# Optimization experiments

Measured on AMD Instinct MI355X. Metric: run time of the kernel, lower is better.

## Reference

```python
import jax, jax.numpy as jnp
import numpy as np

NUM_ITEMS = 100000
HIDDEN = 128
NNZ = 1600000


def setup_inputs() -> dict:
    key = jax.random.key(0)
    k1, k2, k3, k4, k5, k6 = jax.random.split(key, 6)
    item_embedding_table = jax.random.normal(k1, (NUM_ITEMS, HIDDEN), dtype=jnp.float32)
    adj_rows = jnp.sort(jax.random.randint(k2, (NNZ,), 0, NUM_ITEMS, dtype=jnp.int32))
    adj_cols = jax.random.randint(k3, (NNZ,), 0, NUM_ITEMS, dtype=jnp.int32)
    adj_vals = jax.random.uniform(k4, (NNZ,), dtype=jnp.float32)
    # nn.Linear default init (uniform in +-1/sqrt(fan_in)) approximated by scaled normal
    W_weight = jax.random.normal(k5, (HIDDEN, HIDDEN), dtype=jnp.float32) / np.sqrt(HIDDEN)
    W_bias = jax.random.normal(k6, (HIDDEN,), dtype=jnp.float32) * 0.01
    return {
        "item_embedding_table": item_embedding_table,
        "adj_rows": adj_rows,
        "adj_cols": adj_cols,
        "adj_vals": adj_vals,
        "W_weight": W_weight,
        "W_bias": W_bias,
    }


def reference(item_embedding_table, adj_rows, adj_cols, adj_vals, W_weight, W_bias):
    # support = W(x): x @ W^T + b   (nn.Linear convention: weight [out, in])
    support = jnp.einsum("nd,hd->nh", item_embedding_table, W_weight) + W_bias  # [N, H]
    # output = sparse_coo(adj) @ support, via gather + segment-sum scatter
    msgs = adj_vals[:, None] * support[adj_cols]  # [nnz, H]
    output = jax.ops.segment_sum(msgs, adj_rows, num_segments=NUM_ITEMS)  # [N, H]
    return output
```

## Files before the change

### kernel.cpp

```cpp
#include <hip/hip_runtime.h>

#define N_ITEMS 100000
#define HID 128
#define NNZ_T 1600000

typedef unsigned short ushort_t;
typedef unsigned int uint_t;
typedef short bf16x8 __attribute__((ext_vector_type(8)));
typedef float f32x4 __attribute__((ext_vector_type(4)));

static __device__ __forceinline__ ushort_t f32_to_bf16(float f) {
    uint_t u = __float_as_uint(f);
    uint_t r = (u + 0x7FFFu + ((u >> 16) & 1u)) >> 16;
    return (ushort_t)r;
}

__global__ void prep_w(const float* __restrict__ W, ushort_t* __restrict__ Wb) {
    int i = blockIdx.x * blockDim.x + threadIdx.x;
    Wb[i] = f32_to_bf16(W[i]);
}

__global__ void build_rowptr(const int* __restrict__ rows, int* __restrict__ row_ptr) {
    int r = blockIdx.x * blockDim.x + threadIdx.x;
    if (r > N_ITEMS) return;
    int lo = 0, hi = NNZ_T;
    while (lo < hi) {
        int mid = (lo + hi) >> 1;
        if (rows[mid] < r) lo = mid + 1; else hi = mid;
    }
    row_ptr[r] = lo;
}

__global__ __launch_bounds__(256) void gemm_mfma(
    const float* __restrict__ X, const ushort_t* __restrict__ Wb,
    const float* __restrict__ bias, ushort_t* __restrict__ S) {
    const int lane = threadIdx.x & 63;
    const int wave = threadIdx.x >> 6;
    const int m = lane & 15;
    const int q = lane >> 4;
    const int row0 = blockIdx.x * 64 + wave * 16;

    int arow = row0 + m;
    if (arow >= N_ITEMS) arow = N_ITEMS - 1;

    f32x4 acc[8] = {};

#pragma unroll
    for (int kb = 0; kb < 4; ++kb) {
        const int k0 = kb * 32 + q * 8;
        float4 a0 = *(const float4*)&X[(size_t)arow * HID + k0];
        float4 a1 = *(const float4*)&X[(size_t)arow * HID + k0 + 4];
        bf16x8 af;
        af[0] = (short)f32_to_bf16(a0.x); af[1] = (short)f32_to_bf16(a0.y);
        af[2] = (short)f32_to_bf16(a0.z); af[3] = (short)f32_to_bf16(a0.w);
        af[4] = (short)f32_to_bf16(a1.x); af[5] = (short)f32_to_bf16(a1.y);
        af[6] = (short)f32_to_bf16(a1.z); af[7] = (short)f32_to_bf16(a1.w);
#pragma unroll
        for (int nt = 0; nt < 8; ++nt) {
            bf16x8 bfr = *(const bf16x8*)&Wb[(size_t)(nt * 16 + m) * HID + k0];
            acc[nt] = __builtin_amdgcn_mfma_f32_16x16x32_bf16(af, bfr, acc[nt], 0, 0, 0);
        }
    }

#pragma unroll
    for (int nt = 0; nt < 8; ++nt) {
        const int col = nt * 16 + m;
        const float bv = bias[col];
#pragma unroll
        for (int r = 0; r < 4; ++r) {
            const int row = row0 + q * 4 + r;
            if (row < N_ITEMS)
                S[(size_t)row * HID + col] = f32_to_bf16(acc[nt][r] + bv);
        }
    }
}

__global__ __launch_bounds__(256) void spmm_csr(
    const int* __restrict__ cols, const float* __restrict__ vals,
    const int* __restrict__ row_ptr, const ushort_t* __restrict__ S,
    float* __restrict__ out) {
    const int lane = threadIdx.x & 63;
    const int row = blockIdx.x * 4 + (int)__builtin_amdgcn_readfirstlane(threadIdx.x >> 6);
    if (row >= N_ITEMS) return;

    const int p0 = row_ptr[row];
    const int p1 = row_ptr[row + 1];

    float2 acc = make_float2(0.f, 0.f);
    int p = p0;
    for (; p + 8 <= p1; p += 8) {
        uint_t u[8]; float v[8];
#pragma unroll
        for (int j = 0; j < 8; ++j) {
            int c = cols[p + j];
            v[j] = vals[p + j];
            u[j] = *(const uint_t*)&S[(size_t)c * HID + 2 * lane];
        }
#pragma unroll
        for (int j = 0; j < 8; ++j) {
            acc.x = fmaf(v[j], __uint_as_float(u[j] << 16), acc.x);
            acc.y = fmaf(v[j], __uint_as_float(u[j] & 0xFFFF0000u), acc.y);
        }
    }
    for (; p < p1; ++p) {
        int c = cols[p];
        float v = vals[p];
        uint_t u = *(const uint_t*)&S[(size_t)c * HID + 2 * lane];
        acc.x = fmaf(v, __uint_as_float(u << 16), acc.x);
        acc.y = fmaf(v, __uint_as_float(u & 0xFFFF0000u), acc.y);
    }
    *(float2*)&out[(size_t)row * HID + 2 * lane] = acc;
}

extern "C" void kernel_launch(void* const* d_in, const int* in_sizes, int n_in,
                              void* d_out, int out_size, void* d_ws, size_t ws_size,
                              hipStream_t stream) {
    const float* X    = (const float*)d_in[0];
    const int*   rows = (const int*)  d_in[1];
    const int*   cols = (const int*)  d_in[2];
    const float* vals = (const float*)d_in[3];
    const float* W    = (const float*)d_in[4];
    const float* bias = (const float*)d_in[5];
    float* out = (float*)d_out;

    ushort_t* Wb      = (ushort_t*)d_ws;
    ushort_t* S       = Wb + HID * HID;
    int*      row_ptr = (int*)(S + (size_t)N_ITEMS * HID);

    prep_w<<<(HID * HID) / 256, 256, 0, stream>>>(W, Wb);
    build_rowptr<<<(N_ITEMS + 256) / 256, 256, 0, stream>>>(rows, row_ptr);
    gemm_mfma<<<(N_ITEMS + 63) / 64, 256, 0, stream>>>(X, Wb, bias, S);
    spmm_csr<<<(N_ITEMS + 3) / 4, 256, 0, stream>>>(cols, vals, row_ptr, S, out);
}
```

Before: 222.6 us.

## Fuse weight cast and rowptr build into GEMM, process two rows per SpMM wave

Drops the separate W-to-bf16 and row_ptr kernels. The GEMM now converts fp32 W inline, and the binary-search rowptr build runs in extra blocks of the same launch, so two kernels become one. The MFMA operands are swapped so each lane holds contiguous output columns, which lets the epilogue write packed 8-byte stores with a float4 bias load. The SpMM kernel handles two adjacent rows per wave with interleaved, clamped and masked gathers, giving more memory-level parallelism. The cost is redundant W conversion in every GEMM block and wasted gathers when the two row lengths differ.

```diff
diff --git a/kernel.cpp b/kernel.cpp
--- a/kernel.cpp
+++ b/kernel.cpp
@@ -3,6 +3,8 @@
 #define N_ITEMS 100000
 #define HID 128
 #define NNZ_T 1600000
+#define GEMM_BLOCKS 1563
+#define RP_BLOCKS 391
 
 typedef unsigned short ushort_t;
 typedef unsigned int uint_t;
@@ -15,25 +17,23 @@
     return (ushort_t)r;
 }
 
-__global__ void prep_w(const float* __restrict__ W, ushort_t* __restrict__ Wb) {
-    int i = blockIdx.x * blockDim.x + threadIdx.x;
-    Wb[i] = f32_to_bf16(W[i]);
-}
+__global__ __launch_bounds__(256) void gemm_rowptr(
+    const float* __restrict__ X, const float* __restrict__ W,
+    const float* __restrict__ bias, const int* __restrict__ rows,
+    ushort_t* __restrict__ S, int* __restrict__ row_ptr) {
 
-__global__ void build_rowptr(const int* __restrict__ rows, int* __restrict__ row_ptr) {
-    int r = blockIdx.x * blockDim.x + threadIdx.x;
-    if (r > N_ITEMS) return;
-    int lo = 0, hi = NNZ_T;
-    while (lo < hi) {
-        int mid = (lo + hi) >> 1;
-        if (rows[mid] < r) lo = mid + 1; else hi = mid;
+    if (blockIdx.x >= GEMM_BLOCKS) {
+        int r = (blockIdx.x - GEMM_BLOCKS) * 256 + threadIdx.x;
+        if (r > N_ITEMS) return;
+        int lo = 0, hi = NNZ_T;
+        while (lo < hi) {
+            int mid = (lo + hi) >> 1;
+            if (rows[mid] < r) lo = mid + 1; else hi = mid;
+        }
+        row_ptr[r] = lo;
+        return;
     }
-    row_ptr[r] = lo;
-}
 
-__global__ __launch_bounds__(256) void gemm_mfma(
-    const float* __restrict__ X, const ushort_t* __restrict__ Wb,
-    const float* __restrict__ bias, ushort_t* __restrict__ S) {
     const int lane = threadIdx.x & 63;
     const int wave = threadIdx.x >> 6;
     const int m = lane & 15;
@@ -50,28 +50,38 @@
         const int k0 = kb * 32 + q * 8;
         float4 a0 = *(const float4*)&X[(size_t)arow * HID + k0];
         float4 a1 = *(const float4*)&X[(size_t)arow * HID + k0 + 4];
-        bf16x8 af;
-        af[0] = (short)f32_to_bf16(a0.x); af[1] = (short)f32_to_bf16(a0.y);
-        af[2] = (short)f32_to_bf16(a0.z); af[3] = (short)f32_to_bf16(a0.w);
-        af[4] = (short)f32_to_bf16(a1.x); af[5] = (short)f32_to_bf16(a1.y);
-        af[6] = (short)f32_to_bf16(a1.z); af[7] = (short)f32_to_bf16(a1.w);
+        bf16x8 xf;
+        xf[0] = (short)f32_to_bf16(a0.x); xf[1] = (short)f32_to_bf16(a0.y);
+        xf[2] = (short)f32_to_bf16(a0.z); xf[3] = (short)f32_to_bf16(a0.w);
+        xf[4] = (short)f32_to_bf16(a1.x); xf[5] = (short)f32_to_bf16(a1.y);
+        xf[6] = (short)f32_to_bf16(a1.z); xf[7] = (short)f32_to_bf16(a1.w);
 #pragma unroll
         for (int nt = 0; nt < 8; ++nt) {
-            bf16x8 bfr = *(const bf16x8*)&Wb[(size_t)(nt * 16 + m) * HID + k0];
-            acc[nt] = __builtin_amdgcn_mfma_f32_16x16x32_bf16(af, bfr, acc[nt], 0, 0, 0);
+            float4 w0 = *(const float4*)&W[(size_t)(nt * 16 + m) * HID + k0];
+            float4 w1 = *(const float4*)&W[(size_t)(nt * 16 + m) * HID + k0 + 4];
+            bf16x8 wf;
+            wf[0] = (short)f32_to_bf16(w0.x); wf[1] = (short)f32_to_bf16(w0.y);
+            wf[2] = (short)f32_to_bf16(w0.z); wf[3] = (short)f32_to_bf16(w0.w);
+            wf[4] = (short)f32_to_bf16(w1.x); wf[5] = (short)f32_to_bf16(w1.y);
+            wf[6] = (short)f32_to_bf16(w1.z); wf[7] = (short)f32_to_bf16(w1.w);
+            acc[nt] = __builtin_amdgcn_mfma_f32_16x16x32_bf16(wf, xf, acc[nt], 0, 0, 0);
         }
     }
 
+    const int srow = row0 + m;
+    const bool ok = srow < N_ITEMS;
 #pragma unroll
     for (int nt = 0; nt < 8; ++nt) {
-        const int col = nt * 16 + m;
-        const float bv = bias[col];
-#pragma unroll
-        for (int r = 0; r < 4; ++r) {
-            const int row = row0 + q * 4 + r;
-            if (row < N_ITEMS)
-                S[(size_t)row * HID + col] = f32_to_bf16(acc[nt][r] + bv);
-        }
+        const int c0 = nt * 16 + q * 4;
+        float4 bv = *(const float4*)&bias[c0];
+        ushort_t h0 = f32_to_bf16(acc[nt][0] + bv.x);
+        ushort_t h1 = f32_to_bf16(acc[nt][1] + bv.y);
+        ushort_t h2 = f32_to_bf16(acc[nt][2] + bv.z);
+        ushort_t h3 = f32_to_bf16(acc[nt][3] + bv.w);
+        uint2 pk;
+        pk.x = (uint_t)h0 | ((uint_t)h1 << 16);
+        pk.y = (uint_t)h2 | ((uint_t)h3 << 16);
+        if (ok) *(uint2*)&S[(size_t)srow * HID + c0] = pk;
     }
 }
 
@@ -80,36 +90,47 @@
     const int* __restrict__ row_ptr, const ushort_t* __restrict__ S,
     float* __restrict__ out) {
     const int lane = threadIdx.x & 63;
-    const int row = blockIdx.x * 4 + (int)__builtin_amdgcn_readfirstlane(threadIdx.x >> 6);
-    if (row >= N_ITEMS) return;
+    const int wid = blockIdx.x * 4 + ((threadIdx.x >> 6) & 3);
+    const int r0 = wid * 2;
+    if (r0 >= N_ITEMS) return;
 
-    const int p0 = row_ptr[row];
-    const int p1 = row_ptr[row + 1];
+    const int p0 = row_ptr[r0];
+    const int p1 = row_ptr[r0 + 1];
+    const int p2 = row_ptr[r0 + 2];
+    const int la = (p1 > p0) ? p1 - 1 : 0;
+    const int lb = (p2 > p1) ? p2 - 1 : 0;
+    const int nb = max(p1 - p0, p2 - p1);
 
-    float2 acc = make_float2(0.f, 0.f);
-    int p = p0;
-    for (; p + 8 <= p1; p += 8) {
-        uint_t u[8]; float v[8];
+    const uint_t off = 2 * lane;
+    float2 acc0 = make_float2(0.f, 0.f);
+    float2 acc1 = make_float2(0.f, 0.f);
+
+    for (int b = 0; b < nb; b += 8) {
+        uint_t u0[8], u1[8];
+        float v0[8], v1[8];
 #pragma unroll
         for (int j = 0; j < 8; ++j) {
-            int c = cols[p + j];
-            v[j] = vals[p + j];
-            u[j] = *(const uint_t*)&S[(size_t)c * HID + 2 * lane];
+            int ia = p0 + b + j;
+            int ib = p1 + b + j;
+            bool oka = ia < p1, okb = ib < p2;
+            ia = min(ia, la);
+            ib = min(ib, lb);
+            int ca = cols[ia], cb = cols[ib];
+            v0[j] = oka ? vals[ia] : 0.f;
+            v1[j] = okb ? vals[ib] : 0.f;
+            u0[j] = *(const uint_t*)&S[(size_t)ca * HID + off];
+            u1[j] = *(const uint_t*)&S[(size_t)cb * HID + off];
         }
 #pragma unroll
         for (int j = 0; j < 8; ++j) {
-            acc.x = fmaf(v[j], __uint_as_float(u[j] << 16), acc.x);
-            acc.y = fmaf(v[j], __uint_as_float(u[j] & 0xFFFF0000u), acc.y);
+            acc0.x = fmaf(v0[j], __uint_as_float(u0[j] << 16), acc0.x);
+            acc0.y = fmaf(v0[j], __uint_as_float(u0[j] & 0xFFFF0000u), acc0.y);
+            acc1.x = fmaf(v1[j], __uint_as_float(u1[j] << 16), acc1.x);
+            acc1.y = fmaf(v1[j], __uint_as_float(u1[j] & 0xFFFF0000u), acc1.y);
         }
     }
-    for (; p < p1; ++p) {
-        int c = cols[p];
-        float v = vals[p];
-        uint_t u = *(const uint_t*)&S[(size_t)c * HID + 2 * lane];
-        acc.x = fmaf(v, __uint_as_float(u << 16), acc.x);
-        acc.y = fmaf(v, __uint_as_float(u & 0xFFFF0000u), acc.y);
-    }
-    *(float2*)&out[(size_t)row * HID + 2 * lane] = acc;
+    *(float2*)&out[(size_t)r0 * HID + off] = acc0;
+    *(float2*)&out[(size_t)(r0 + 1) * HID + off] = acc1;
 }
 
 extern "C" void kernel_launch(void* const* d_in, const int* in_sizes, int n_in,
@@ -123,12 +144,9 @@
     const float* bias = (const float*)d_in[5];
     float* out = (float*)d_out;
 
-    ushort_t* Wb      = (ushort_t*)d_ws;
-    ushort_t* S       = Wb + HID * HID;
+    ushort_t* S       = (ushort_t*)d_ws;
     int*      row_ptr = (int*)(S + (size_t)N_ITEMS * HID);
 
-    prep_w<<<(HID * HID) / 256, 256, 0, stream>>>(W, Wb);
-    build_rowptr<<<(N_ITEMS + 256) / 256, 256, 0, stream>>>(rows, row_ptr);
-    gemm_mfma<<<(N_ITEMS + 63) / 64, 256, 0, stream>>>(X, Wb, bias, S);
-    spmm_csr<<<(N_ITEMS + 3) / 4, 256, 0, stream>>>(cols, vals, row_ptr, S, out);
+    gemm_rowptr<<<GEMM_BLOCKS + RP_BLOCKS, 256, 0, stream>>>(X, W, bias, rows, S, row_ptr);
+    spmm_csr<<<(N_ITEMS / 2 + 3) / 4, 256, 0, stream>>>(cols, vals, row_ptr, S, out);
 }
```

Measured after the change: 259.3 us. 1.17x slower.
